# Performance work log

Hardware: AMD Instinct MI355X
Metric: run time of the kernel (lower is better)

## Reference

```python
import jax, jax.numpy as jnp
import numpy as np

B, C, H, W = 2, 96, 40, 40
DIN, N, R, K = 192, 16, 6, 4  # d_inner, d_state, dt_rank, k_group


def silu(x):
    return x * jax.nn.sigmoid(x)


def dwconv3x3(x, w, b):
    # depthwise 3x3, SAME padding; w: (DIN,1,3,3)
    y = jax.lax.conv_general_dilated(x, w, (1, 1), [(1, 1), (1, 1)],
                                     feature_group_count=x.shape[1])
    return y + b[None, :, None, None]


def cross_scan(x):
    # (B,C,H,W) -> (B,4,C,L): row-major, col-major, and their reverses
    b, c, h, w = x.shape
    x0 = x.reshape(b, c, h * w)
    x1 = x.transpose(0, 1, 3, 2).reshape(b, c, h * w)
    return jnp.stack([x0, x1, x0[..., ::-1], x1[..., ::-1]], axis=1)


def cross_merge(y, h, w):
    # (B,4,C,H,W) -> (B,C,L)
    b, k, c = y.shape[0], y.shape[1], y.shape[2]
    y = y.reshape(b, k, c, h * w)
    y = y[:, :2] + y[:, 2:][..., ::-1]
    y1 = y[:, 1].reshape(b, c, w, h).transpose(0, 1, 3, 2).reshape(b, c, h * w)
    return y[:, 0] + y1


def selective_scan(u, dt, A, Bm, Cm, Dv, dbias):
    # u, dt: (B,K,DIN,L); A: (K*DIN,N); Bm, Cm: (B,K,N,L); Dv: (K*DIN,); dbias: (K*DIN,)
    b, k, d, l = u.shape
    n = A.shape[1]
    A4 = A.reshape(k, d, n)
    dt = jax.nn.softplus(dt + dbias.reshape(1, k, d, 1))
    # discretize: dA = exp(dt*A), dBu = dt*B*u  -> shapes (B,K,D,L,N)
    dA = jnp.exp(dt[..., None] * A4[None, :, :, None, :])
    dBu = dt[..., None] * Bm.transpose(0, 1, 3, 2)[:, :, None, :, :] * u[..., None]

    def combine(c1, c2):
        a1, b1 = c1
        a2, b2 = c2
        return a1 * a2, a2 * b1 + b2

    _, h = jax.lax.associative_scan(combine, (dA, dBu), axis=3)  # h: (B,K,D,L,N)
    y = jnp.einsum('bkdln,bknl->bkdl', h, Cm)
    return y + Dv.reshape(1, k, d, 1) * u


def ln2d(x, g, b):
    # LayerNorm over channel dim (channel_first LayerNorm2d)
    mu = x.mean(axis=1, keepdims=True)
    var = jnp.mean((x - mu) ** 2, axis=1, keepdims=True)
    xn = (x - mu) / jnp.sqrt(var + 1e-5)
    return xn * g[None, :, None, None] + b[None, :, None, None]


def setup_inputs():
    key = jax.random.key(0)
    ks = jax.random.split(key, 24)

    def rn(k, shape, s=0.02):
        return jax.random.normal(k, shape, dtype=jnp.float32) * s

    A_log = jnp.tile(jnp.log(jnp.arange(1, N + 1, dtype=jnp.float32))[None, :], (K * DIN, 1))
    return {
        'x_rgb': jax.random.normal(ks[0], (B, C, H, W), jnp.float32),
        'x_e': jax.random.normal(ks[1], (B, C, H, W), jnp.float32),
        'in_proj_w': rn(ks[2], (DIN, C)),
        'in_proj_mx_w': rn(ks[3], (DIN, C)),
        'conv_w': rn(ks[4], (DIN, 1, 3, 3), 0.1),
        'conv_b': jnp.zeros((DIN,), jnp.float32),
        'xproj1_w': rn(ks[5], (K, R + 2 * N, DIN)),
        'xproj2_w': rn(ks[6], (K, R + 2 * N, DIN)),
        'dtproj1_w': rn(ks[7], (K, DIN, R), 0.1),
        'dtproj1_b': rn(ks[8], (K, DIN), 0.1) - 4.0,
        'dtproj2_w': rn(ks[9], (K, DIN, R), 0.1),
        'dtproj2_b': rn(ks[10], (K, DIN), 0.1) - 4.0,
        'A_log_1': A_log,
        'A_log_2': A_log,
        'D_1': jnp.ones((K * DIN,), jnp.float32),
        'D_2': jnp.ones((K * DIN,), jnp.float32),
        'norm1_g': jnp.ones((DIN,), jnp.float32),
        'norm1_b': jnp.zeros((DIN,), jnp.float32),
        'norm2_g': jnp.ones((DIN,), jnp.float32),
        'norm2_b': jnp.zeros((DIN,), jnp.float32),
        'fc1_w1': rn(ks[11], (DIN // 16, DIN), 0.05),
        'fc1_w2': rn(ks[12], (DIN, DIN // 16), 0.05),
        'fc2_w1': rn(ks[13], (DIN // 16, DIN), 0.05),
        'fc2_w2': rn(ks[14], (DIN, DIN // 16), 0.05),
        'out_proj_w': rn(ks[15], (C, 2 * DIN)),
    }


def reference(x_rgb, x_e, in_proj_w, in_proj_mx_w, conv_w, conv_b, xproj1_w, xproj2_w,
              dtproj1_w, dtproj1_b, dtproj2_w, dtproj2_b, A_log_1, A_log_2, D_1, D_2,
              norm1_g, norm1_b, norm2_g, norm2_b, fc1_w1, fc1_w2, fc2_w1, fc2_w2, out_proj_w):
    # in_proj (1x1 conv style Linear2d)
    xr = jnp.einsum('oc,bchw->bohw', in_proj_w, x_rgb)
    xe = jnp.einsum('oc,bchw->bohw', in_proj_mx_w, x_e)
    # shared depthwise conv + SiLU
    xr = silu(dwconv3x3(xr, conv_w, conv_b))
    xe = silu(dwconv3x3(xe, conv_w, conv_b))
    b, d, h, w = xr.shape

    xs_r = cross_scan(xr)  # (B,K,DIN,L)
    xs_e = cross_scan(xe)

    def proj(xs, xp_w, dt_w):
        t = jnp.einsum('bkdl,kcd->bkcl', xs, xp_w)  # grouped 1x1 conv1d
        dts, Bm, Cm = jnp.split(t, [R, R + N], axis=2)
        dts = jnp.einsum('bkrl,kdr->bkdl', dts, dt_w)
        return dts, Bm, Cm

    d_r, B_r, C_r = proj(xs_r, xproj1_w, dtproj1_w)
    d_e, B_e, C_e = proj(xs_e, xproj2_w, dtproj2_w)

    # cross attention: rgb scan consumes C and D of the other modality
    y_r = selective_scan(xs_r, d_r, -jnp.exp(A_log_1), B_r, C_e, D_2, dtproj1_b.reshape(-1))
    y_e = selective_scan(xs_e, d_e, -jnp.exp(A_log_2), B_e, C_r, D_1, dtproj2_b.reshape(-1))

    y_r = cross_merge(y_r.reshape(b, K, d, h, w), h, w).reshape(b, d, h, w)
    y_e = cross_merge(y_e.reshape(b, K, d, h, w), h, w).reshape(b, d, h, w)
    y_r = ln2d(y_r, norm1_g, norm1_b)
    y_e = ln2d(y_e, norm2_g, norm2_b)

    # cross squeeze-excitation
    sq_r = xr.mean(axis=(2, 3))
    sq_e = xe.mean(axis=(2, 3))
    exc_r = jax.nn.sigmoid(silu(sq_r @ fc1_w1.T) @ fc1_w2.T)
    exc_e = jax.nn.sigmoid(silu(sq_e @ fc2_w1.T) @ fc2_w2.T)
    y_r = y_r * exc_e[:, :, None, None]
    y_e = y_e * exc_r[:, :, None, None]

    y = jnp.concatenate([y_r, y_e], axis=1)  # (B, 2*DIN, H, W)
    return jnp.einsum('oc,bchw->bohw', out_proj_w, y)
```

## Files before the change

### kernel.cpp

```cpp
#include <hip/hip_runtime.h>
#include <math.h>

#define BN   2
#define CIN  96
#define HH   40
#define WW   40
#define LL   1600
#define DIN  192
#define NS   16
#define RR   6
#define KK   4
#define CH   25

typedef _Float16 h16;

__device__ __forceinline__ float sigmoidf_(float x){ return 1.0f/(1.0f+expf(-x)); }
__device__ __forceinline__ float softplus_fast(float x){
  return x > 20.0f ? x : __logf(1.0f + __expf(x));
}

__device__ __forceinline__ void pow_tree(float R, float* p){
  float R2 = R * R;
  float R4 = R2 * R2;
  float R8 = R4 * R4;
  p[0]  = R;        p[1]  = R2;       p[2]  = R2 * R;   p[3]  = R4;
  p[4]  = R4 * R;   p[5]  = R4 * R2;  p[6]  = R4 * p[2];p[7]  = R8;
  p[8]  = R8 * R;   p[9]  = R8 * R2;  p[10] = R8 * p[2];p[11] = R8 * R4;
  p[12] = R8 * p[4];p[13] = R8 * p[5];p[14] = R8 * p[6];p[15] = R8 * R8;
}

__device__ __forceinline__ void unpack8(float4 v, float* dst){
  const h16* hp = reinterpret_cast<const h16*>(&v);
  #pragma unroll
  for (int i = 0; i < 8; ++i) dst[i] = (float)hp[i];
}

__global__ void k_inproj(const float* __restrict__ x_rgb, const float* __restrict__ x_e,
                         const float* __restrict__ w_rgb, const float* __restrict__ w_e,
                         h16* __restrict__ xproj){
  __shared__ float xin[8][100];
  int l0 = blockIdx.x * 8;
  int mb = blockIdx.y;
  int m = mb / BN, b = mb % BN;
  const float* xsrc = (m == 0 ? x_rgb : x_e) + (size_t)b * CIN * LL;
  const float* w    = (m == 0 ? w_rgb : w_e);
  for (int idx = threadIdx.x; idx < CIN * 8; idx += 256){
    int c = idx >> 3, px = idx & 7;
    xin[px][c] = xsrc[c * LL + l0 + px];
  }
  __syncthreads();
  int px = threadIdx.x & 7;
  int o0 = (threadIdx.x >> 3) * 6;
  float acc[6];
  #pragma unroll
  for (int i = 0; i < 6; ++i) acc[i] = 0.f;
  const float4* xv = reinterpret_cast<const float4*>(xin[px]);
  for (int cc = 0; cc < CIN / 4; ++cc){
    float4 x4 = xv[cc];
    #pragma unroll
    for (int i = 0; i < 6; ++i){
      float4 w4 = *reinterpret_cast<const float4*>(w + (o0 + i) * CIN + cc * 4);
      acc[i] += w4.x * x4.x + w4.y * x4.y + w4.z * x4.z + w4.w * x4.w;
    }
  }
  #pragma unroll
  for (int i = 0; i < 6; ++i)
    xproj[((size_t)mb * DIN + o0 + i) * LL + l0 + px] = (h16)acc[i];
}

__global__ void k_conv(const h16* __restrict__ xproj, const float* __restrict__ conv_w,
                       const float* __restrict__ conv_b, h16* __restrict__ x_act,
                       h16* __restrict__ x_actT, h16* __restrict__ u_chA,
                       h16* __restrict__ u_chT, float* __restrict__ sq){
  __shared__ float pl[LL];
  __shared__ float sact[LL + HH];
  __shared__ float red[4];
  int d  = blockIdx.x;
  int mb = blockIdx.y;
  const h16* src = xproj + ((size_t)mb * DIN + d) * LL;
  for (int p = threadIdx.x; p < LL; p += blockDim.x) pl[p] = (float)src[p];
  __syncthreads();
  float cw[9];
  #pragma unroll
  for (int j = 0; j < 9; ++j) cw[j] = conv_w[d * 9 + j];
  float bias = conv_b[d];
  h16* dst = x_act + ((size_t)mb * DIN + d) * LL;
  float lsum = 0.f;
  for (int p = threadIdx.x; p < LL; p += blockDim.x){
    int py = p / WW, px = p % WW;
    float acc = bias;
    #pragma unroll
    for (int dy = -1; dy <= 1; ++dy){
      int yy = py + dy;
      if (yy < 0 || yy >= HH) continue;
      #pragma unroll
      for (int dx = -1; dx <= 1; ++dx){
        int xx = px + dx;
        if (xx < 0 || xx >= WW) continue;
        acc += cw[(dy + 1) * 3 + (dx + 1)] * pl[yy * WW + xx];
      }
    }
    float s = acc * sigmoidf_(acc);
    dst[p] = (h16)s;
    sact[p + p / WW] = s;
    lsum += s;
  }
  #pragma unroll
  for (int off = 32; off; off >>= 1) lsum += __shfl_down(lsum, off);
  if ((threadIdx.x & 63) == 0) red[threadIdx.x >> 6] = lsum;
  __syncthreads();
  if (threadIdx.x == 0)
    sq[mb * DIN + d] = (red[0] + red[1] + red[2] + red[3]) * (1.0f / LL);
  size_t po = ((size_t)mb * DIN + d) * LL;
  h16* dstT = x_actT + po;
  h16* uA   = u_chA + po;
  h16* uT   = u_chT + po;
  for (int q = threadIdx.x; q < LL; q += blockDim.x){
    int lt = (q % WW) * WW + q / WW;
    dstT[q] = (h16)sact[lt + lt / WW];
    int l = (q & 63) * CH + (q >> 6);
    uA[q] = (h16)sact[l + l / WW];
    int pt = (l % WW) * WW + l / WW;
    uT[q] = (h16)sact[pt + pt / WW];
  }
}

__global__ void k_xproj(const h16* __restrict__ x_act, const h16* __restrict__ x_actT,
                        const float* __restrict__ xp1, const float* __restrict__ xp2,
                        const float* __restrict__ dtw1, const float* __restrict__ dtb1,
                        const float* __restrict__ dtw2, const float* __restrict__ dtb2,
                        h16* __restrict__ B_ch, h16* __restrict__ C_ch,
                        h16* __restrict__ dsp_all){
  __shared__ h16 xs[DIN][64];
  __shared__ float td[RR][64];
  int l0 = blockIdx.x * 64;
  int k  = blockIdx.y >> 1;
  int hf = blockIdx.y & 1;
  int mb = blockIdx.z; int m = mb / BN;
  const float* xw = (m == 0 ? xp1 : xp2) + k * 38 * DIN;
  const h16* xa = ((k & 1) ? x_actT : x_act) + (size_t)mb * DIN * LL;
  bool rev = (k >= 2);
  for (int idx = threadIdx.x; idx < DIN * 64; idx += 256){
    int dd = idx >> 6, sl = idx & 63;
    int l = l0 + sl; if (rev) l = LL - 1 - l;
    xs[dd][sl] = xa[(size_t)dd * LL + l];
  }
  __syncthreads();
  int ll = threadIdx.x & 63;
  int g  = __builtin_amdgcn_readfirstlane(threadIdx.x >> 6);
  int c0 = (hf * 4 + g) * 5;
  float acc[5];
  #pragma unroll
  for (int i = 0; i < 5; ++i) acc[i] = 0.f;
  for (int dd = 0; dd < DIN; ++dd){
    float xv = (float)xs[dd][ll];
    #pragma unroll
    for (int i = 0; i < 5; ++i){
      int cc = c0 + i; if (cc > 37) cc = 37;
      acc[i] += xw[cc * DIN + dd] * xv;
    }
  }
  int mbk = mb * KK + k;
  int lq = l0 + ll;
  int q = (lq % CH) * 64 + lq / CH;
  int nc = 38 - c0; if (nc > 5) nc = 5;
  for (int i = 0; i < nc; ++i){
    int c = c0 + i;
    float v = acc[i];
    if (c < RR){
      td[c][ll] = v;
    } else if (c < RR + NS){
      int n = c - RR;
      B_ch[(((size_t)mbk * 2 + (n >> 3)) * LL + q) * 8 + (n & 7)] = (h16)v;
    } else {
      int n = c - RR - NS;
      C_ch[(((size_t)mbk * 2 + (n >> 3)) * LL + q) * 8 + (n & 7)] = (h16)v;
    }
  }
  if (hf == 0){
    __syncthreads();
    const float* dtw = (m == 0 ? dtw1 : dtw2);
    const float* dtb = (m == 0 ? dtb1 : dtb2);
    h16* dsp = dsp_all + (size_t)mbk * DIN * LL;
    for (int idx = threadIdx.x; idx < DIN * 64; idx += 256){
      int dd = __builtin_amdgcn_readfirstlane(idx >> 6);
      int px = idx & 63;
      int kd = k * DIN + dd;
      const float* w = dtw + kd * RR;
      float a = dtb[kd];
      #pragma unroll
      for (int r = 0; r < RR; ++r) a += w[r] * td[r][px];
      dsp[(size_t)dd * LL + l0 + px] = (h16)softplus_fast(a);
    }
  }
}

__global__ void __launch_bounds__(256, 3) k_scan(
    const h16* __restrict__ u_chA, const h16* __restrict__ u_chT,
    const h16* __restrict__ dsp_all, const h16* __restrict__ B_ch,
    const h16* __restrict__ C_ch,
    const float* __restrict__ Alog1, const float* __restrict__ Alog2,
    const float* __restrict__ D1, const float* __restrict__ D2,
    h16* __restrict__ y_px){
  __shared__ h16 ysth[4][LL];
  __shared__ h16 dtl[4][LL];
  int wv   = threadIdx.x >> 6;
  int lane = threadIdx.x & 63;
  int chain = blockIdx.x * 4 + wv;
  int d   = chain % DIN;
  int mbk = chain / DIN;
  int k   = mbk % KK;
  int mb  = mbk / KK;
  int m = mb / BN, b = mb % BN;
  int kd = k * DIN + d;
  bool rev = (k >= 2);

  const float* Alog = (m == 0 ? Alog1 : Alog2) + kd * NS;
  float An[NS];
  bool fastA = true;
  #pragma unroll
  for (int n = 0; n < NS; ++n){
    An[n] = -__expf(Alog[n]);
    fastA = fastA && (fabsf(An[n] + (float)(n + 1)) <= 1e-4f * (float)(n + 1));
  }
  float Dv = (m == 0 ? D2 : D1)[kd];

  const h16* dsp_row = dsp_all + (size_t)chain * LL;
  {
    const h16* src = dsp_row + lane * CH;
    #pragma unroll
    for (int i = 0; i < CH; ++i)
      dtl[wv][i * 64 + lane] = src[i];
  }

  const float4* B0 = reinterpret_cast<const float4*>(B_ch) + (size_t)mbk * 2 * LL;
  int mbk_o = ((1 - m) * BN + b) * KK + k;
  const float4* C0 = reinterpret_cast<const float4*>(C_ch) + (size_t)mbk_o * 2 * LL;
  const h16* urow = ((k & 1) ? u_chT : u_chA) + ((size_t)mb * DIN + d) * LL;

  float h[NS];
  #pragma unroll
  for (int n = 0; n < NS; ++n) h[n] = 0.f;
  float Sdt = 0.f;

  if (fastA){
    float4 bA0, bA1, cA0, cA1, bB0, bB1, cB0, cB1;
    float uA_, uB_, dtA_, dtB_;
    {
      int qa = lane;
      dtA_ = (float)dtl[wv][qa];
      uA_  = (float)urow[rev ? (LL - 1 - qa) : qa];
      bA0 = B0[qa]; bA1 = B0[LL + qa];
      cA0 = C0[qa]; cA1 = C0[LL + qa];
      int qb = 64 + lane;
      dtB_ = (float)dtl[wv][qb];
      uB_  = (float)urow[rev ? (LL - 1 - qb) : qb];
      bB0 = B0[qb]; bB1 = B0[LL + qb];
      cB0 = C0[qb]; cB1 = C0[LL + qb];
    }
    for (int s = 0; s < CH - 1; s += 2){
      {
        float dt = dtA_, u = uA_;
        float4 b0 = bA0, b1 = bA1, c0 = cA0, c1 = cA1;
        if (s + 2 < CH){
          int q2 = (s + 2) * 64 + lane;
          dtA_ = (float)dtl[wv][q2];
          uA_  = (float)urow[rev ? (LL - 1 - q2) : q2];
          bA0 = B0[q2]; bA1 = B0[LL + q2];
          cA0 = C0[q2]; cA1 = C0[LL + q2];
        }
        Sdt += dt;
        float du = dt * u;
        float Bv[NS], Cv[NS];
        unpack8(b0, Bv); unpack8(b1, Bv + 8);
        unpack8(c0, Cv); unpack8(c1, Cv + 8);
        float p[NS];
        pow_tree(__expf(-dt), p);
        float y0 = Dv * u, y1 = 0.f, y2 = 0.f, y3 = 0.f;
        #pragma unroll
        for (int n = 0; n < NS; ++n){
          h[n] = p[n] * h[n] + du * Bv[n];
          float t = h[n] * Cv[n];
          if      ((n & 3) == 0) y0 += t;
          else if ((n & 3) == 1) y1 += t;
          else if ((n & 3) == 2) y2 += t;
          else                   y3 += t;
        }
        ysth[wv][lane * CH + s] = (h16)((y0 + y1) + (y2 + y3));
      }
      {
        float dt = dtB_, u = uB_;
        float4 b0 = bB0, b1 = bB1, c0 = cB0, c1 = cB1;
        if (s + 3 < CH){
          int q3 = (s + 3) * 64 + lane;
          dtB_ = (float)dtl[wv][q3];
          uB_  = (float)urow[rev ? (LL - 1 - q3) : q3];
          bB0 = B0[q3]; bB1 = B0[LL + q3];
          cB0 = C0[q3]; cB1 = C0[LL + q3];
        }
        Sdt += dt;
        float du = dt * u;
        float Bv[NS], Cv[NS];
        unpack8(b0, Bv); unpack8(b1, Bv + 8);
        unpack8(c0, Cv); unpack8(c1, Cv + 8);
        float p[NS];
        pow_tree(__expf(-dt), p);
        float y0 = Dv * u, y1 = 0.f, y2 = 0.f, y3 = 0.f;
        #pragma unroll
        for (int n = 0; n < NS; ++n){
          h[n] = p[n] * h[n] + du * Bv[n];
          float t = h[n] * Cv[n];
          if      ((n & 3) == 0) y0 += t;
          else if ((n & 3) == 1) y1 += t;
          else if ((n & 3) == 2) y2 += t;
          else                   y3 += t;
        }
        ysth[wv][lane * CH + s + 1] = (h16)((y0 + y1) + (y2 + y3));
      }
    }
    {
      const int s = CH - 1;
      float dt = dtA_, u = uA_;
      Sdt += dt;
      float du = dt * u;
      float Bv[NS], Cv[NS];
      unpack8(bA0, Bv); unpack8(bA1, Bv + 8);
      unpack8(cA0, Cv); unpack8(cA1, Cv + 8);
      float p[NS];
      pow_tree(__expf(-dt), p);
      float y0 = Dv * u, y1 = 0.f, y2 = 0.f, y3 = 0.f;
      #pragma unroll
      for (int n = 0; n < NS; ++n){
        h[n] = p[n] * h[n] + du * Bv[n];
        float t = h[n] * Cv[n];
        if      ((n & 3) == 0) y0 += t;
        else if ((n & 3) == 1) y1 += t;
        else if ((n & 3) == 2) y2 += t;
        else                   y3 += t;
      }
      ysth[wv][lane * CH + s] = (h16)((y0 + y1) + (y2 + y3));
    }
  } else {
    #pragma unroll 5
    for (int s = 0; s < CH; ++s){
      int q = s * 64 + lane;
      float dt = (float)dtl[wv][q];
      Sdt += dt;
      float u  = (float)urow[rev ? (LL - 1 - q) : q];
      float du = dt * u;
      float Bv[NS], Cv[NS];
      unpack8(B0[q], Bv); unpack8(B0[LL + q], Bv + 8);
      unpack8(C0[q], Cv); unpack8(C0[LL + q], Cv + 8);
      float y0 = Dv * u, y1 = 0.f, y2 = 0.f, y3 = 0.f;
      #pragma unroll
      for (int n = 0; n < NS; ++n){
        float dA = __expf(dt * An[n]);
        h[n] = dA * h[n] + du * Bv[n];
        float t = h[n] * Cv[n];
        if      ((n & 3) == 0) y0 += t;
        else if ((n & 3) == 1) y1 += t;
        else if ((n & 3) == 2) y2 += t;
        else                   y3 += t;
      }
      ysth[wv][lane * CH + s] = (h16)((y0 + y1) + (y2 + y3));
    }
  }
  float aP[NS];
  if (fastA){
    pow_tree(__expf(-Sdt), aP);
  } else {
    #pragma unroll
    for (int n = 0; n < NS; ++n) aP[n] = __expf(Sdt * An[n]);
  }

  #pragma unroll
  for (int off = 1; off < 64; off <<= 1){
    #pragma unroll
    for (int n = 0; n < NS; ++n){
      float ap = __shfl_up(aP[n], off);
      float bp = __shfl_up(h[n],  off);
      if (lane >= off){
        h[n]  = aP[n] * bp + h[n];
        aP[n] = aP[n] * ap;
      }
    }
  }
  #pragma unroll
  for (int n = 0; n < NS; ++n){
    float v = __shfl_up(h[n], 1);
    h[n] = (lane == 0) ? 0.f : v;
  }

  if (fastA){
    float4 cA0, cA1, cB0, cB1;
    float dtA_, dtB_;
    {
      int qa = lane;
      dtA_ = (float)dtl[wv][qa];
      cA0 = C0[qa]; cA1 = C0[LL + qa];
      int qb = 64 + lane;
      dtB_ = (float)dtl[wv][qb];
      cB0 = C0[qb]; cB1 = C0[LL + qb];
    }
    float cum = 0.f;
    for (int s = 0; s < CH - 1; s += 2){
      {
        float dt = dtA_;
        float4 c0 = cA0, c1 = cA1;
        if (s + 2 < CH){
          int q2 = (s + 2) * 64 + lane;
          dtA_ = (float)dtl[wv][q2];
          cA0 = C0[q2]; cA1 = C0[LL + q2];
        }
        cum += dt;
        float Rc = __expf(-cum);
        float Cv[NS];
        unpack8(c0, Cv); unpack8(c1, Cv + 8);
        float p[NS];
        pow_tree(Rc, p);
        float s0 = 0.f, s1 = 0.f, s2 = 0.f, s3 = 0.f;
        #pragma unroll
        for (int n = 0; n < NS; ++n){
          float t = h[n] * p[n] * Cv[n];
          if      ((n & 3) == 0) s0 += t;
          else if ((n & 3) == 1) s1 += t;
          else if ((n & 3) == 2) s2 += t;
          else                   s3 += t;
        }
        int li = lane * CH + s;
        ysth[wv][li] = (h16)((float)ysth[wv][li] + (s0 + s1) + (s2 + s3));
      }
      {
        float dt = dtB_;
        float4 c0 = cB0, c1 = cB1;
        if (s + 3 < CH){
          int q3 = (s + 3) * 64 + lane;
          dtB_ = (float)dtl[wv][q3];
          cB0 = C0[q3]; cB1 = C0[LL + q3];
        }
        cum += dt;
        float Rc = __expf(-cum);
        float Cv[NS];
        unpack8(c0, Cv); unpack8(c1, Cv + 8);
        float p[NS];
        pow_tree(Rc, p);
        float s0 = 0.f, s1 = 0.f, s2 = 0.f, s3 = 0.f;
        #pragma unroll
        for (int n = 0; n < NS; ++n){
          float t = h[n] * p[n] * Cv[n];
          if      ((n & 3) == 0) s0 += t;
          else if ((n & 3) == 1) s1 += t;
          else if ((n & 3) == 2) s2 += t;
          else                   s3 += t;
        }
        int li = lane * CH + s + 1;
        ysth[wv][li] = (h16)((float)ysth[wv][li] + (s0 + s1) + (s2 + s3));
      }
    }
    {
      const int s = CH - 1;
      cum += dtA_;
      float Rc = __expf(-cum);
      float Cv[NS];
      unpack8(cA0, Cv); unpack8(cA1, Cv + 8);
      float p[NS];
      pow_tree(Rc, p);
      float s0 = 0.f, s1 = 0.f, s2 = 0.f, s3 = 0.f;
      #pragma unroll
      for (int n = 0; n < NS; ++n){
        float t = h[n] * p[n] * Cv[n];
        if      ((n & 3) == 0) s0 += t;
        else if ((n & 3) == 1) s1 += t;
        else if ((n & 3) == 2) s2 += t;
        else                   s3 += t;
      }
      int li = lane * CH + s;
      ysth[wv][li] = (h16)((float)ysth[wv][li] + (s0 + s1) + (s2 + s3));
    }
  } else {
    float cum = 0.f;
    #pragma unroll 5
    for (int s = 0; s < CH; ++s){
      int q = s * 64 + lane;
      cum += (float)dtl[wv][q];
      float Cv[NS];
      unpack8(C0[q], Cv); unpack8(C0[LL + q], Cv + 8);
      float s0 = 0.f, s1 = 0.f, s2 = 0.f, s3 = 0.f;
      #pragma unroll
      for (int n = 0; n < NS; ++n){
        float t = h[n] * __expf(cum * An[n]) * Cv[n];
        if      ((n & 3) == 0) s0 += t;
        else if ((n & 3) == 1) s1 += t;
        else if ((n & 3) == 2) s2 += t;
        else                   s3 += t;
      }
      int li = lane * CH + s;
      ysth[wv][li] = (h16)((float)ysth[wv][li] + (s0 + s1) + (s2 + s3));
    }
  }

  h16* yo = y_px + (size_t)chain * LL;
  for (int qq = lane; qq < LL; qq += 64){
    int l;
    if      (k == 0) l = qq;
    else if (k == 1) l = (qq % WW) * WW + qq / WW;
    else if (k == 2) l = LL - 1 - qq;
    else             { int qt = (qq % WW) * WW + qq / WW; l = LL - 1 - qt; }
    yo[qq] = ysth[wv][l];
  }
}

__global__ void __launch_bounds__(256) k_mergeout(
    const h16* __restrict__ y_px, const float* __restrict__ sq,
    const float* __restrict__ fc1_w1, const float* __restrict__ fc1_w2,
    const float* __restrict__ fc2_w1, const float* __restrict__ fc2_w2,
    const float* __restrict__ n1g, const float* __restrict__ n1b,
    const float* __restrict__ n2g, const float* __restrict__ n2b,
    const float* __restrict__ wout, float* __restrict__ out){
  __shared__ float acc[2 * DIN][5];
  __shared__ float yt[4][388];
  __shared__ float ps[2][4][32], ps2[2][4][32];
  __shared__ float mu_s[2][4], inv_s[2][4];
  __shared__ float sqs[2][DIN];
  __shared__ float hid[2][12];
  __shared__ float exc_s[2][DIN];
  int p0 = blockIdx.x * 4;
  int b  = blockIdx.y;
  int tid = threadIdx.x;
  for (int idx = tid; idx < 2 * DIN * 4; idx += 256){
    int pp = idx & 3, row = idx >> 2;
    int mm = (row >= DIN), dd = row - mm * DIN;
    const h16* yb = y_px + ((size_t)(mm * BN + b) * KK * DIN + dd) * LL + p0 + pp;
    acc[row][pp] = (float)yb[0] + (float)yb[(size_t)DIN * LL]
                 + (float)yb[2 * (size_t)DIN * LL] + (float)yb[3 * (size_t)DIN * LL];
  }
  for (int i = tid; i < 2 * DIN; i += 256){
    int mm = (i >= DIN), dd = i - mm * DIN;
    sqs[mm][dd] = sq[((1 - mm) * BN + b) * DIN + dd];
  }
  __syncthreads();
  if (tid < 24){
    int mm = tid / 12, j = tid - mm * 12;
    const float* w1 = (mm == 1 ? fc1_w1 : fc2_w1);
    float a = 0.f;
    for (int cch = 0; cch < DIN; ++cch) a += w1[j * DIN + cch] * sqs[mm][cch];
    hid[mm][j] = a * sigmoidf_(a);
  }
  {
    int pp = tid & 3, mm = (tid >> 2) & 1, g = tid >> 3;
    float s = 0.f, s2 = 0.f;
    #pragma unroll
    for (int j = 0; j < 6; ++j){
      float v = acc[mm * DIN + g * 6 + j][pp];
      s += v; s2 += v * v;
    }
    ps[mm][pp][g] = s; ps2[mm][pp][g] = s2;
  }
  __syncthreads();
  if (tid < 8){
    int mm = tid >> 2, pp = tid & 3;
    float s = 0.f, s2 = 0.f;
    #pragma unroll
    for (int g = 0; g < 32; ++g){ s += ps[mm][pp][g]; s2 += ps2[mm][pp][g]; }
    float mu  = s * (1.0f / DIN);
    float var = s2 * (1.0f / DIN) - mu * mu;
    mu_s[mm][pp] = mu; inv_s[mm][pp] = rsqrtf(var + 1e-5f);
  }
  for (int i = tid; i < 2 * DIN; i += 256){
    int mm = (i >= DIN), dd = i - mm * DIN;
    const float* w2 = (mm == 1 ? fc1_w2 : fc2_w2);
    float e = 0.f;
    #pragma unroll
    for (int j = 0; j < 12; ++j) e += w2[dd * 12 + j] * hid[mm][j];
    exc_s[mm][dd] = sigmoidf_(e);
  }
  __syncthreads();
  for (int idx = tid; idx < 2 * DIN * 4; idx += 256){
    int pp = idx & 3, row = idx >> 2;
    int mm = (row >= DIN), dd = row - mm * DIN;
    float g  = (mm ? n2g : n1g)[dd];
    float bb = (mm ? n2b : n1b)[dd];
    float v = (acc[row][pp] - mu_s[mm][pp]) * inv_s[mm][pp] * g + bb;
    yt[pp][row] = v * exc_s[mm][dd];
  }
  __syncthreads();
  int pp = tid & 3;
  int og = tid >> 2;
  const float4* yv = reinterpret_cast<const float4*>(yt[pp]);
  float a0 = 0.f, a1 = 0.f;
  if (og < 32){
    for (int cc = 0; cc < 96; ++cc){
      float4 x4 = yv[cc];
      float4 w40 = *reinterpret_cast<const float4*>(wout + og * 2 * DIN + cc * 4);
      float4 w41 = *reinterpret_cast<const float4*>(wout + (og + 64) * 2 * DIN + cc * 4);
      a0 += w40.x * x4.x + w40.y * x4.y + w40.z * x4.z + w40.w * x4.w;
      a1 += w41.x * x4.x + w41.y * x4.y + w41.z * x4.z + w41.w * x4.w;
    }
    out[((size_t)b * CIN + og) * LL + p0 + pp] = a0;
    out[((size_t)b * CIN + og + 64) * LL + p0 + pp] = a1;
  } else {
    for (int cc = 0; cc < 96; ++cc){
      float4 x4 = yv[cc];
      float4 w40 = *reinterpret_cast<const float4*>(wout + og * 2 * DIN + cc * 4);
      a0 += w40.x * x4.x + w40.y * x4.y + w40.z * x4.z + w40.w * x4.w;
    }
    out[((size_t)b * CIN + og) * LL + p0 + pp] = a0;
  }
}

extern "C" void kernel_launch(void* const* d_in, const int* in_sizes, int n_in,
                              void* d_out, int out_size, void* d_ws, size_t ws_size,
                              hipStream_t stream){
  const float* x_rgb   = (const float*)d_in[0];
  const float* x_e     = (const float*)d_in[1];
  const float* in_w    = (const float*)d_in[2];
  const float* in_mx_w = (const float*)d_in[3];
  const float* conv_w  = (const float*)d_in[4];
  const float* conv_b  = (const float*)d_in[5];
  const float* xp1     = (const float*)d_in[6];
  const float* xp2     = (const float*)d_in[7];
  const float* dtw1    = (const float*)d_in[8];
  const float* dtb1    = (const float*)d_in[9];
  const float* dtw2    = (const float*)d_in[10];
  const float* dtb2    = (const float*)d_in[11];
  const float* Alog1   = (const float*)d_in[12];
  const float* Alog2   = (const float*)d_in[13];
  const float* D1      = (const float*)d_in[14];
  const float* D2      = (const float*)d_in[15];
  const float* n1g     = (const float*)d_in[16];
  const float* n1b     = (const float*)d_in[17];
  const float* n2g     = (const float*)d_in[18];
  const float* n2b     = (const float*)d_in[19];
  const float* fc1_w1  = (const float*)d_in[20];
  const float* fc1_w2  = (const float*)d_in[21];
  const float* fc2_w1  = (const float*)d_in[22];
  const float* fc2_w2  = (const float*)d_in[23];
  const float* wout    = (const float*)d_in[24];

  float* ws = (float*)d_ws;
  h16*   u_chA   = (h16*)(ws);
  h16*   u_chT   = (h16*)(ws + 614400);
  h16*   x_act   = (h16*)(ws + 1228800);
  h16*   x_actT  = (h16*)(ws + 1843200);
  h16*   xproj   = (h16*)(ws + 2457600);
  h16*   y_px    = (h16*)(ws + 3686400);
  h16*   B_ch    = (h16*)(ws + 8601600);
  h16*   C_ch    = (h16*)(ws + 8806400);
  h16*   dsp     = (h16*)(ws + 9011200);
  float* sq      = ws + 11468800;

  k_inproj  <<<dim3(LL / 8, 2 * BN), 256, 0, stream>>>(x_rgb, x_e, in_w, in_mx_w, xproj);
  k_conv    <<<dim3(DIN, 2 * BN), 256, 0, stream>>>(xproj, conv_w, conv_b,
                                                    x_act, x_actT, u_chA, u_chT, sq);
  k_xproj   <<<dim3(LL / 64, KK * 2, 2 * BN), 256, 0, stream>>>(x_act, x_actT, xp1, xp2,
                                                                dtw1, dtb1, dtw2, dtb2,
                                                                B_ch, C_ch, dsp);
  k_scan    <<<768, 256, 0, stream>>>(u_chA, u_chT, dsp, B_ch, C_ch,
                                      Alog1, Alog2, D1, D2, y_px);
  k_mergeout<<<dim3(LL / 4, BN), 256, 0, stream>>>(y_px, sq,
                                                   fc1_w1, fc1_w2, fc2_w1, fc2_w2,
                                                   n1g, n1b, n2g, n2b,
                                                   wout, (float*)d_out);
}
```

Before: 140.9 us.

## Feed xproj from chunk-permuted u buffers and write dt directly in scan order

```diff
diff --git a/kernel.cpp b/kernel.cpp
--- a/kernel.cpp
+++ b/kernel.cpp
@@ -69,8 +69,7 @@
 }
 
 __global__ void k_conv(const h16* __restrict__ xproj, const float* __restrict__ conv_w,
-                       const float* __restrict__ conv_b, h16* __restrict__ x_act,
-                       h16* __restrict__ x_actT, h16* __restrict__ u_chA,
+                       const float* __restrict__ conv_b, h16* __restrict__ u_chA,
                        h16* __restrict__ u_chT, float* __restrict__ sq){
   __shared__ float pl[LL];
   __shared__ float sact[LL + HH];
@@ -84,7 +83,6 @@
   #pragma unroll
   for (int j = 0; j < 9; ++j) cw[j] = conv_w[d * 9 + j];
   float bias = conv_b[d];
-  h16* dst = x_act + ((size_t)mb * DIN + d) * LL;
   float lsum = 0.f;
   for (int p = threadIdx.x; p < LL; p += blockDim.x){
     int py = p / WW, px = p % WW;
@@ -101,7 +99,6 @@
       }
     }
     float s = acc * sigmoidf_(acc);
-    dst[p] = (h16)s;
     sact[p + p / WW] = s;
     lsum += s;
   }
@@ -112,12 +109,9 @@
   if (threadIdx.x == 0)
     sq[mb * DIN + d] = (red[0] + red[1] + red[2] + red[3]) * (1.0f / LL);
   size_t po = ((size_t)mb * DIN + d) * LL;
-  h16* dstT = x_actT + po;
-  h16* uA   = u_chA + po;
-  h16* uT   = u_chT + po;
+  h16* uA = u_chA + po;
+  h16* uT = u_chT + po;
   for (int q = threadIdx.x; q < LL; q += blockDim.x){
-    int lt = (q % WW) * WW + q / WW;
-    dstT[q] = (h16)sact[lt + lt / WW];
     int l = (q & 63) * CH + (q >> 6);
     uA[q] = (h16)sact[l + l / WW];
     int pt = (l % WW) * WW + l / WW;
@@ -125,7 +119,7 @@
   }
 }
 
-__global__ void k_xproj(const h16* __restrict__ x_act, const h16* __restrict__ x_actT,
+__global__ void k_xproj(const h16* __restrict__ u_chA, const h16* __restrict__ u_chT,
                         const float* __restrict__ xp1, const float* __restrict__ xp2,
                         const float* __restrict__ dtw1, const float* __restrict__ dtb1,
                         const float* __restrict__ dtw2, const float* __restrict__ dtb2,
@@ -133,17 +127,18 @@
                         h16* __restrict__ dsp_all){
   __shared__ h16 xs[DIN][64];
   __shared__ float td[RR][64];
-  int l0 = blockIdx.x * 64;
+  int bx = blockIdx.x;
   int k  = blockIdx.y >> 1;
   int hf = blockIdx.y & 1;
   int mb = blockIdx.z; int m = mb / BN;
   const float* xw = (m == 0 ? xp1 : xp2) + k * 38 * DIN;
-  const h16* xa = ((k & 1) ? x_actT : x_act) + (size_t)mb * DIN * LL;
+  const h16* xa = ((k & 1) ? u_chT : u_chA) + (size_t)mb * DIN * LL;
   bool rev = (k >= 2);
+  int qrbase = rev ? ((24 - bx) * 64) : (bx * 64);
   for (int idx = threadIdx.x; idx < DIN * 64; idx += 256){
     int dd = idx >> 6, sl = idx & 63;
-    int l = l0 + sl; if (rev) l = LL - 1 - l;
-    xs[dd][sl] = xa[(size_t)dd * LL + l];
+    int qr = rev ? (qrbase + 63 - sl) : (qrbase + sl);
+    xs[dd][sl] = xa[(size_t)dd * LL + qr];
   }
   __syncthreads();
   int ll = threadIdx.x & 63;
@@ -161,8 +156,7 @@
     }
   }
   int mbk = mb * KK + k;
-  int lq = l0 + ll;
-  int q = (lq % CH) * 64 + lq / CH;
+  int q = bx * 64 + ll;
   int nc = 38 - c0; if (nc > 5) nc = 5;
   for (int i = 0; i < nc; ++i){
     int c = c0 + i;
@@ -190,7 +184,7 @@
       float a = dtb[kd];
       #pragma unroll
       for (int r = 0; r < RR; ++r) a += w[r] * td[r][px];
-      dsp[(size_t)dd * LL + l0 + px] = (h16)softplus_fast(a);
+      dsp[(size_t)dd * LL + bx * 64 + px] = (h16)softplus_fast(a);
     }
   }
 }
@@ -203,7 +197,6 @@
     const float* __restrict__ D1, const float* __restrict__ D2,
     h16* __restrict__ y_px){
   __shared__ h16 ysth[4][LL];
-  __shared__ h16 dtl[4][LL];
   int wv   = threadIdx.x >> 6;
   int lane = threadIdx.x & 63;
   int chain = blockIdx.x * 4 + wv;
@@ -226,13 +219,6 @@
   float Dv = (m == 0 ? D2 : D1)[kd];
 
   const h16* dsp_row = dsp_all + (size_t)chain * LL;
-  {
-    const h16* src = dsp_row + lane * CH;
-    #pragma unroll
-    for (int i = 0; i < CH; ++i)
-      dtl[wv][i * 64 + lane] = src[i];
-  }
-
   const float4* B0 = reinterpret_cast<const float4*>(B_ch) + (size_t)mbk * 2 * LL;
   int mbk_o = ((1 - m) * BN + b) * KK + k;
   const float4* C0 = reinterpret_cast<const float4*>(C_ch) + (size_t)mbk_o * 2 * LL;
@@ -248,12 +234,12 @@
     float uA_, uB_, dtA_, dtB_;
     {
       int qa = lane;
-      dtA_ = (float)dtl[wv][qa];
+      dtA_ = (float)dsp_row[qa];
       uA_  = (float)urow[rev ? (LL - 1 - qa) : qa];
       bA0 = B0[qa]; bA1 = B0[LL + qa];
       cA0 = C0[qa]; cA1 = C0[LL + qa];
       int qb = 64 + lane;
-      dtB_ = (float)dtl[wv][qb];
+      dtB_ = (float)dsp_row[qb];
       uB_  = (float)urow[rev ? (LL - 1 - qb) : qb];
       bB0 = B0[qb]; bB1 = B0[LL + qb];
       cB0 = C0[qb]; cB1 = C0[LL + qb];
@@ -264,7 +250,7 @@
         float4 b0 = bA0, b1 = bA1, c0 = cA0, c1 = cA1;
         if (s + 2 < CH){
           int q2 = (s + 2) * 64 + lane;
-          dtA_ = (float)dtl[wv][q2];
+          dtA_ = (float)dsp_row[q2];
           uA_  = (float)urow[rev ? (LL - 1 - q2) : q2];
           bA0 = B0[q2]; bA1 = B0[LL + q2];
           cA0 = C0[q2]; cA1 = C0[LL + q2];
@@ -293,7 +279,7 @@
         float4 b0 = bB0, b1 = bB1, c0 = cB0, c1 = cB1;
         if (s + 3 < CH){
           int q3 = (s + 3) * 64 + lane;
-          dtB_ = (float)dtl[wv][q3];
+          dtB_ = (float)dsp_row[q3];
           uB_  = (float)urow[rev ? (LL - 1 - q3) : q3];
           bB0 = B0[q3]; bB1 = B0[LL + q3];
           cB0 = C0[q3]; cB1 = C0[LL + q3];
@@ -344,7 +330,7 @@
     #pragma unroll 5
     for (int s = 0; s < CH; ++s){
       int q = s * 64 + lane;
-      float dt = (float)dtl[wv][q];
+      float dt = (float)dsp_row[q];
       Sdt += dt;
       float u  = (float)urow[rev ? (LL - 1 - q) : q];
       float du = dt * u;
@@ -396,10 +382,10 @@
     float dtA_, dtB_;
     {
       int qa = lane;
-      dtA_ = (float)dtl[wv][qa];
+      dtA_ = (float)dsp_row[qa];
       cA0 = C0[qa]; cA1 = C0[LL + qa];
       int qb = 64 + lane;
-      dtB_ = (float)dtl[wv][qb];
+      dtB_ = (float)dsp_row[qb];
       cB0 = C0[qb]; cB1 = C0[LL + qb];
     }
     float cum = 0.f;
@@ -409,7 +395,7 @@
         float4 c0 = cA0, c1 = cA1;
         if (s + 2 < CH){
           int q2 = (s + 2) * 64 + lane;
-          dtA_ = (float)dtl[wv][q2];
+          dtA_ = (float)dsp_row[q2];
           cA0 = C0[q2]; cA1 = C0[LL + q2];
         }
         cum += dt;
@@ -435,7 +421,7 @@
         float4 c0 = cB0, c1 = cB1;
         if (s + 3 < CH){
           int q3 = (s + 3) * 64 + lane;
-          dtB_ = (float)dtl[wv][q3];
+          dtB_ = (float)dsp_row[q3];
           cB0 = C0[q3]; cB1 = C0[LL + q3];
         }
         cum += dt;
@@ -482,7 +468,7 @@
     #pragma unroll 5
     for (int s = 0; s < CH; ++s){
       int q = s * 64 + lane;
-      cum += (float)dtl[wv][q];
+      cum += (float)dsp_row[q];
       float Cv[NS];
       unpack8(C0[q], Cv); unpack8(C0[LL + q], Cv + 8);
       float s0 = 0.f, s1 = 0.f, s2 = 0.f, s3 = 0.f;
@@ -640,8 +626,6 @@
   float* ws = (float*)d_ws;
   h16*   u_chA   = (h16*)(ws);
   h16*   u_chT   = (h16*)(ws + 614400);
-  h16*   x_act   = (h16*)(ws + 1228800);
-  h16*   x_actT  = (h16*)(ws + 1843200);
   h16*   xproj   = (h16*)(ws + 2457600);
   h16*   y_px    = (h16*)(ws + 3686400);
   h16*   B_ch    = (h16*)(ws + 8601600);
@@ -651,10 +635,10 @@
 
   k_inproj  <<<dim3(LL / 8, 2 * BN), 256, 0, stream>>>(x_rgb, x_e, in_w, in_mx_w, xproj);
   k_conv    <<<dim3(DIN, 2 * BN), 256, 0, stream>>>(xproj, conv_w, conv_b,
-                                                    x_act, x_actT, u_chA, u_chT, sq);
-  k_xproj   <<<dim3(LL / 64, KK * 2, 2 * BN), 256, 0, stream>>>(x_act, x_actT, xp1, xp2,
-                                                                dtw1, dtb1, dtw2, dtb2,
-                                                                B_ch, C_ch, dsp);
+                                                    u_chA, u_chT, sq);
+  k_xproj   <<<dim3(25, KK * 2, 2 * BN), 256, 0, stream>>>(u_chA, u_chT, xp1, xp2,
+                                                           dtw1, dtb1, dtw2, dtb2,
+                                                           B_ch, C_ch, dsp);
   k_scan    <<<768, 256, 0, stream>>>(u_chA, u_chT, dsp, B_ch, C_ch,
                                       Alog1, Alog2, D1, D2, y_px);
   k_mergeout<<<dim3(LL / 4, BN), 256, 0, stream>>>(y_px, sq,
```

New measurement: 140.1 us, median of 2. About the same (-0.5%).
